# Kernel optimization log

Measured on AMD Instinct MI355X. Metric: run time of the kernel, lower is better.

The kernel has to match this reference:

```python
import jax, jax.numpy as jnp
import numpy as np

B, S, D, H = 2, 2048, 1024, 16
HD = D // H
DFF = 4 * D
EPS = 1e-5


def layernorm(x, g, b):
    mu = jnp.mean(x, axis=-1, keepdims=True)
    var = jnp.mean((x - mu) ** 2, axis=-1, keepdims=True)
    return (x - mu) * jax.lax.rsqrt(var + EPS) * g + b


def setup_inputs() -> dict:
    key = jax.random.key(0)
    ks = jax.random.split(key, 16)
    sc = 0.02
    return {
        "x": jax.random.normal(ks[0], (B, S, D), jnp.float32),
        "pos_emb": jax.random.normal(ks[1], (S, D), jnp.float32),
        "ln1_g": jnp.ones((D,), jnp.float32),
        "ln1_b": jnp.zeros((D,), jnp.float32),
        "w_qkv": jax.random.normal(ks[2], (D, 3 * D), jnp.float32) * sc,
        "b_qkv": jnp.zeros((3 * D,), jnp.float32),
        "w_o": jax.random.normal(ks[3], (D, D), jnp.float32) * sc,
        "b_o": jnp.zeros((D,), jnp.float32),
        "ln2_g": jnp.ones((D,), jnp.float32),
        "ln2_b": jnp.zeros((D,), jnp.float32),
        "w_fc": jax.random.normal(ks[4], (D, DFF), jnp.float32) * sc,
        "b_fc": jnp.zeros((DFF,), jnp.float32),
        "w_proj": jax.random.normal(ks[5], (DFF, D), jnp.float32) * sc,
        "b_proj": jnp.zeros((D,), jnp.float32),
    }


def reference(x, pos_emb, ln1_g, ln1_b, w_qkv, b_qkv, w_o, b_o,
              ln2_g, ln2_b, w_fc, b_fc, w_proj, b_proj):
    # --- attention sub-block: x + attn(norm1(x) + pos_emb) ---
    h = layernorm(x, ln1_g, ln1_b) + pos_emb  # [B,S,D]
    qkv = h @ w_qkv + b_qkv                    # [B,S,3D]
    qkv = qkv.reshape(B, S, 3, H, HD).transpose(2, 0, 3, 1, 4)  # [3,B,H,S,HD]
    q, k, v = qkv[0], qkv[1], qkv[2]
    # naive full attention: materialize [B,H,S,S]
    w = jnp.einsum('bhqd,bhkd->bhqk', q, k) / jnp.sqrt(jnp.float32(HD))
    causal = jnp.tril(jnp.ones((S, S), bool))  # True = keep
    w = jnp.where(causal, w, -jnp.inf)
    a = jax.nn.softmax(w, axis=-1)
    out = jnp.einsum('bhqk,bhkd->bhqd', a, v)   # [B,H,S,HD]
    out = out.transpose(0, 2, 1, 3).reshape(B, S, D)
    x = x + out @ w_o + b_o
    # --- MLP sub-block: x + mlp(norm2(x)) ---
    m = layernorm(x, ln2_g, ln2_b)
    m = jax.nn.gelu(m @ w_fc + b_fc) @ w_proj + b_proj
    return x + m
```

## Files before the change

kernel.cpp:

```cpp
#include <hip/hip_runtime.h>
#include <hip/hip_bf16.h>

typedef __hip_bfloat16 bf16_t;
typedef __bf16 bf16x8 __attribute__((ext_vector_type(8)));
typedef float f32x4 __attribute__((ext_vector_type(4)));

__device__ __forceinline__ void gload_lds16(const void* g, void* l) {
  __builtin_amdgcn_global_load_lds(
      (const __attribute__((address_space(1))) void*)g,
      (__attribute__((address_space(3))) void*)l, 16, 0, 0);
}

__device__ __forceinline__ unsigned short f2bf(float f) {
  bf16_t h = __float2bfloat16(f);
  return reinterpret_cast<unsigned short&>(h);
}

__global__ __launch_bounds__(256) void wtrans_kernel(
    const float* __restrict__ in, bf16_t* __restrict__ out, int K, int N) {
  __shared__ float tile[32][33];
  int tx = threadIdx.x, ty = threadIdx.y;
  int n = blockIdx.x * 32 + tx;
  int k0 = blockIdx.y * 32 + ty;
#pragma unroll
  for (int j = 0; j < 32; j += 8) tile[ty + j][tx] = in[(size_t)(k0 + j) * N + n];
  __syncthreads();
  int k = blockIdx.y * 32 + tx;
  int n0 = blockIdx.x * 32 + ty;
#pragma unroll
  for (int j = 0; j < 32; j += 8)
    out[(size_t)(n0 + j) * K + k] = __float2bfloat16(tile[tx][ty + j]);
}

__global__ __launch_bounds__(256) void ln_kernel(
    const float* __restrict__ x, const float* __restrict__ g,
    const float* __restrict__ b, const float* __restrict__ pos,
    bf16_t* __restrict__ out, int S) {
  int row = blockIdx.x;
  int tid = threadIdx.x;
  const float4* xr = (const float4*)(x + (size_t)row * 1024);
  float4 v = xr[tid];
  float s1 = v.x + v.y + v.z + v.w;
  float s2 = v.x * v.x + v.y * v.y + v.z * v.z + v.w * v.w;
#pragma unroll
  for (int off = 1; off < 64; off <<= 1) {
    s1 += __shfl_xor(s1, off);
    s2 += __shfl_xor(s2, off);
  }
  __shared__ float red[2][4];
  int w = tid >> 6;
  if ((tid & 63) == 0) { red[0][w] = s1; red[1][w] = s2; }
  __syncthreads();
  s1 = red[0][0] + red[0][1] + red[0][2] + red[0][3];
  s2 = red[1][0] + red[1][1] + red[1][2] + red[1][3];
  float mu = s1 * (1.f / 1024.f);
  float var = s2 * (1.f / 1024.f) - mu * mu;
  float rs = rsqrtf(var + 1e-5f);
  float4 gg = ((const float4*)g)[tid];
  float4 bb = ((const float4*)b)[tid];
  float4 pp = {0.f, 0.f, 0.f, 0.f};
  if (pos) pp = ((const float4*)(pos + (size_t)(row & (S - 1)) * 1024))[tid];
  ushort4 o4;
  o4.x = f2bf((v.x - mu) * rs * gg.x + bb.x + pp.x);
  o4.y = f2bf((v.y - mu) * rs * gg.y + bb.y + pp.y);
  o4.z = f2bf((v.z - mu) * rs * gg.z + bb.z + pp.z);
  o4.w = f2bf((v.w - mu) * rs * gg.w + bb.w + pp.w);
  ((ushort4*)(out + (size_t)row * 1024))[tid] = o4;
}

template <int EPI, int DBUF>
__global__ __launch_bounds__(256) void gemm_bt(
    const bf16_t* __restrict__ A, const bf16_t* __restrict__ BT,
    const float* __restrict__ bias, const float* __restrict__ resid,
    float* __restrict__ outf, bf16_t* __restrict__ outb,
    bf16_t* __restrict__ qb, bf16_t* __restrict__ kb, bf16_t* __restrict__ vb,
    int M, int N, int K) {
  __shared__ char lds[DBUF ? 65536 : 32768];
  int tid = threadIdx.x;
  int l = tid & 63;
  int w = tid >> 6;
  int wr = w >> 1, wc = w & 1;
  int ll = l & 15, lg = l >> 4;
  int chunk = gridDim.x >> 3;
  int swz = (blockIdx.x & 7) * chunk + (blockIdx.x >> 3);
  int nbx = N >> 7;
  int bx = swz % nbx, by = swz / nbx;
  int rowBase = by * 128, colBase = bx * 128;

  f32x4 acc[4][4];
  f32x4 z = {0.f, 0.f, 0.f, 0.f};
#pragma unroll
  for (int i = 0; i < 4; i++)
#pragma unroll
    for (int j = 0; j < 4; j++) acc[i][j] = z;

  auto STAGE = [&](int kt, int c) {
#pragma unroll
    for (int i = 0; i < 4; i++) {
      int p = i * 4096 + tid * 16;
      int o = p ^ (((p >> 7) & 7) << 4);
      int r = o >> 7, cc = (o & 127) >> 1;
      gload_lds16(A + (size_t)(rowBase + r) * K + kt * 64 + cc, lds + c * 32768 + p);
    }
#pragma unroll
    for (int i = 0; i < 4; i++) {
      int p = i * 4096 + tid * 16;
      int o = p ^ (((p >> 7) & 7) << 4);
      int r = o >> 7, cc = (o & 127) >> 1;
      gload_lds16(BT + (size_t)(colBase + r) * K + kt * 64 + cc,
                  lds + c * 32768 + 16384 + p);
    }
  };

  int nkt = K >> 6;
  if (DBUF) STAGE(0, 0);
  int cbuf = 0;
  for (int kt = 0; kt < nkt; ++kt) {
    if (DBUF) {
      __builtin_amdgcn_s_barrier();
      if (kt + 1 < nkt) {
        STAGE(kt + 1, cbuf ^ 1);
        asm volatile("s_waitcnt vmcnt(8)" ::: "memory");
      } else {
        asm volatile("s_waitcnt vmcnt(0)" ::: "memory");
      }
      __builtin_amdgcn_s_barrier();
      asm volatile("" ::: "memory");
    } else {
      __syncthreads();
      STAGE(kt, 0);
      __syncthreads();
    }
    char* Ab = lds + cbuf * 32768;
    char* Bb = Ab + 16384;

    bf16x8 af[4][2], bfv[4][2];
#pragma unroll
    for (int mi = 0; mi < 4; mi++) {
      int row = wr * 64 + mi * 16 + ll;
#pragma unroll
      for (int kk = 0; kk < 2; kk++) {
        int o = (row << 7) + (kk << 6) + (lg << 4);
        af[mi][kk] = *(const bf16x8*)(Ab + (o ^ ((row & 7) << 4)));
      }
    }
#pragma unroll
    for (int ni = 0; ni < 4; ni++) {
      int row = wc * 64 + ni * 16 + ll;
#pragma unroll
      for (int kk = 0; kk < 2; kk++) {
        int o = (row << 7) + (kk << 6) + (lg << 4);
        bfv[ni][kk] = *(const bf16x8*)(Bb + (o ^ ((row & 7) << 4)));
      }
    }
#pragma unroll
    for (int mi = 0; mi < 4; mi++)
#pragma unroll
      for (int ni = 0; ni < 4; ni++)
#pragma unroll
        for (int kk = 0; kk < 2; kk++)
          acc[mi][ni] = __builtin_amdgcn_mfma_f32_16x16x32_bf16(
              af[mi][kk], bfv[ni][kk], acc[mi][ni], 0, 0, 0);
    if (DBUF) cbuf ^= 1;
  }

#pragma unroll
  for (int mi = 0; mi < 4; mi++) {
#pragma unroll
    for (int ni = 0; ni < 4; ni++) {
#pragma unroll
      for (int j = 0; j < 4; j++) {
        int grow = rowBase + wr * 64 + mi * 16 + lg * 4 + j;
        int gcol = colBase + wc * 64 + ni * 16 + ll;
        float v = acc[mi][ni][j] + bias[gcol];
        if (EPI == 0) {
          int bb = grow >> 11, s = grow & 2047;
          int t = gcol >> 10, rem = gcol & 1023;
          int h = rem >> 6, d = rem & 63;
          size_t bh = (size_t)(bb * 16 + h);
          if (t == 0)
            qb[(bh * 2048 + s) * 64 + d] = __float2bfloat16(v);
          else if (t == 1)
            kb[(bh * 2048 + s) * 64 + d] = __float2bfloat16(v);
          else
            vb[(bh * 64 + d) * 2048 + s] = __float2bfloat16(v);
        } else if (EPI == 1) {
          size_t idx = (size_t)grow * N + gcol;
          outf[idx] = resid[idx] + v;
        } else {
          float c3 = v * v * v;
          float t = tanhf(0.7978845608028654f * (v + 0.044715f * c3));
          outb[(size_t)grow * N + gcol] = __float2bfloat16(0.5f * v * (1.f + t));
        }
      }
    }
  }
}

__global__ __launch_bounds__(256, 2) void attn_kernel(
    const bf16_t* __restrict__ qb, const bf16_t* __restrict__ kb,
    const bf16_t* __restrict__ vbT, bf16_t* __restrict__ op, int S) {
  int id = blockIdx.x;
  int bh = id & 31;
  int qt = 15 - (id >> 5);
  int tid = threadIdx.x;
  int w = tid >> 6, l = tid & 63;
  int ll = l & 15, lg = l >> 4;
  __shared__ char lds[49152];
  char* Pw = lds + 32768 + w * 4096;

  int qbase = qt * 128;
  int qlo = qbase + w * 32;
  int qhi = qlo + 31;

  bf16x8 qf[2][2];
#pragma unroll
  for (int mi = 0; mi < 2; mi++) {
    const bf16_t* qrp = qb + ((size_t)bh * S + qbase + w * 32 + mi * 16 + ll) * 64;
#pragma unroll
    for (int kk = 0; kk < 2; kk++) qf[mi][kk] = *(const bf16x8*)(qrp + kk * 32 + lg * 8);
  }

  f32x4 Oacc[2][4];
  f32x4 z = {0.f, 0.f, 0.f, 0.f};
#pragma unroll
  for (int mi = 0; mi < 2; mi++)
#pragma unroll
    for (int i = 0; i < 4; i++) Oacc[mi][i] = z;
  float mrow[2], lrow[2];
#pragma unroll
  for (int mi = 0; mi < 2; mi++) { mrow[mi] = -INFINITY; lrow[mi] = 0.f; }

  int last = 2 * qt + 1;

  auto STAGE = [&](int kt, int c) {
    char* Kt = lds + c * 8192;
    char* Vt = lds + 16384 + c * 8192;
#pragma unroll
    for (int i = 0; i < 2; ++i) {
      int p = i * 4096 + tid * 16;
      int o = p ^ (((p >> 7) & 7) << 4);
      int r = o >> 7, cc = (o & 127) >> 1;
      gload_lds16(kb + ((size_t)bh * S + kt * 64 + r) * 64 + cc, Kt + p);
    }
#pragma unroll
    for (int i = 0; i < 2; ++i) {
      int p = i * 4096 + tid * 16;
      int o = p ^ (((p >> 7) & 7) << 4);
      int d = o >> 7, cc = (o & 127) >> 1;
      gload_lds16(vbT + ((size_t)bh * 64 + d) * S + kt * 64 + cc, Vt + p);
    }
  };

  STAGE(0, 0);
  int c = 0;
  for (int kt = 0; kt <= last; ++kt) {
    __builtin_amdgcn_s_barrier();
    if (kt < last) {
      STAGE(kt + 1, c ^ 1);
      asm volatile("s_waitcnt vmcnt(4)" ::: "memory");
    } else {
      asm volatile("s_waitcnt vmcnt(0)" ::: "memory");
    }
    __builtin_amdgcn_s_barrier();
    asm volatile("" ::: "memory");

    if (kt * 64 <= qhi) {
      char* Kt = lds + c * 8192;
      char* Vt = lds + 16384 + c * 8192;

      bf16x8 kf[4][2];
#pragma unroll
      for (int f = 0; f < 4; f++) {
        int row = f * 16 + ll;
#pragma unroll
        for (int kk = 0; kk < 2; kk++) {
          int o = (row << 7) + (kk << 6) + (lg << 4);
          kf[f][kk] = *(const bf16x8*)(Kt + (o ^ ((row & 7) << 4)));
        }
      }
      f32x4 sfr[2][4];
      __builtin_amdgcn_s_setprio(1);
#pragma unroll
      for (int mi = 0; mi < 2; mi++)
#pragma unroll
        for (int f = 0; f < 4; f++) {
          sfr[mi][f] = z;
#pragma unroll
          for (int kk = 0; kk < 2; kk++)
            sfr[mi][f] = __builtin_amdgcn_mfma_f32_16x16x32_bf16(
                kf[f][kk], qf[mi][kk], sfr[mi][f], 0, 0, 0);
        }
      __builtin_amdgcn_s_setprio(0);

      bool diag = (kt * 64 + 63) > qlo;
      float mx[2];
#pragma unroll
      for (int mi = 0; mi < 2; mi++) {
        int gq = qlo + mi * 16 + ll;
        float m_ = -INFINITY;
#pragma unroll
        for (int f = 0; f < 4; f++)
#pragma unroll
          for (int j = 0; j < 4; j++) {
            float s = sfr[mi][f][j] * 0.125f;
            if (diag && (kt * 64 + f * 16 + lg * 4 + j) > gq) s = -INFINITY;
            sfr[mi][f][j] = s;
            m_ = fmaxf(m_, s);
          }
        m_ = fmaxf(m_, __shfl_xor(m_, 16));
        m_ = fmaxf(m_, __shfl_xor(m_, 32));
        mx[mi] = m_;
      }

      bool ok = (mx[0] <= mrow[0] + 8.f) && (mx[1] <= mrow[1] + 8.f);
      if (!__all(ok)) {
#pragma unroll
        for (int mi = 0; mi < 2; mi++) {
          float mnew = fmaxf(mrow[mi], mx[mi]);
          float fj = __expf(mrow[mi] - mnew);
          mrow[mi] = mnew;
          lrow[mi] *= fj;
#pragma unroll
          for (int j = 0; j < 4; j++) {
            float frow = __shfl(fj, (lg << 2) + j);
#pragma unroll
            for (int fd = 0; fd < 4; fd++) Oacc[mi][fd][j] *= frow;
          }
        }
      }

#pragma unroll
      for (int mi = 0; mi < 2; mi++) {
        float sum = 0.f;
        int q = mi * 16 + ll;
#pragma unroll
        for (int f = 0; f < 4; f++) {
          float p0 = __expf(sfr[mi][f][0] - mrow[mi]);
          float p1 = __expf(sfr[mi][f][1] - mrow[mi]);
          float p2 = __expf(sfr[mi][f][2] - mrow[mi]);
          float p3 = __expf(sfr[mi][f][3] - mrow[mi]);
          sum += (p0 + p1) + (p2 + p3);
          uint2 pk;
          pk.x = (unsigned)f2bf(p0) | ((unsigned)f2bf(p1) << 16);
          pk.y = (unsigned)f2bf(p2) | ((unsigned)f2bf(p3) << 16);
          int o = (q << 7) + ((f * 16 + lg * 4) << 1);
          *(uint2*)(Pw + (o ^ ((q & 7) << 4))) = pk;
        }
        sum += __shfl_xor(sum, 16);
        sum += __shfl_xor(sum, 32);
        lrow[mi] += sum;
      }

      bf16x8 vf2[4][2];
#pragma unroll
      for (int fd = 0; fd < 4; fd++) {
        int row = fd * 16 + ll;
#pragma unroll
        for (int kk = 0; kk < 2; kk++) {
          int o = (row << 7) + (kk << 6) + (lg << 4);
          vf2[fd][kk] = *(const bf16x8*)(Vt + (o ^ ((row & 7) << 4)));
        }
      }
      bf16x8 pf[2][2];
#pragma unroll
      for (int mi = 0; mi < 2; mi++) {
        int pr = mi * 16 + ll;
#pragma unroll
        for (int kk = 0; kk < 2; kk++) {
          int o = (pr << 7) + (kk << 6) + (lg << 4);
          pf[mi][kk] = *(const bf16x8*)(Pw + (o ^ ((pr & 7) << 4)));
        }
      }
      __builtin_amdgcn_s_setprio(1);
#pragma unroll
      for (int mi = 0; mi < 2; mi++)
#pragma unroll
        for (int fd = 0; fd < 4; fd++)
#pragma unroll
          for (int kk = 0; kk < 2; kk++)
            Oacc[mi][fd] = __builtin_amdgcn_mfma_f32_16x16x32_bf16(
                pf[mi][kk], vf2[fd][kk], Oacc[mi][fd], 0, 0, 0);
      __builtin_amdgcn_s_setprio(0);
    }
    c ^= 1;
  }

  int b = bh >> 4, hh = bh & 15;
#pragma unroll
  for (int mi = 0; mi < 2; mi++) {
    float invA = 1.f / lrow[mi];
#pragma unroll
    for (int j = 0; j < 4; j++) {
      float inv = __shfl(invA, (lg << 2) + j);
      int srow = qbase + w * 32 + mi * 16 + lg * 4 + j;
#pragma unroll
      for (int fd = 0; fd < 4; fd++) {
        int col = (hh << 6) + (fd << 4) + ll;
        op[((size_t)b * S + srow) * 1024 + col] = __float2bfloat16(Oacc[mi][fd][j] * inv);
      }
    }
  }
}

extern "C" void kernel_launch(void* const* d_in, const int* in_sizes, int n_in,
                              void* d_out, int out_size, void* d_ws, size_t ws_size,
                              hipStream_t stream) {
  const float* x = (const float*)d_in[0];
  const float* pos_emb = (const float*)d_in[1];
  const float* ln1_g = (const float*)d_in[2];
  const float* ln1_b = (const float*)d_in[3];
  const float* w_qkv = (const float*)d_in[4];
  const float* b_qkv = (const float*)d_in[5];
  const float* w_o = (const float*)d_in[6];
  const float* b_o = (const float*)d_in[7];
  const float* ln2_g = (const float*)d_in[8];
  const float* ln2_b = (const float*)d_in[9];
  const float* w_fc = (const float*)d_in[10];
  const float* b_fc = (const float*)d_in[11];
  const float* w_proj = (const float*)d_in[12];
  const float* b_proj = (const float*)d_in[13];

  char* ws = (char*)d_ws;
  auto take = [&](size_t bytes) {
    char* p = ws;
    ws += (bytes + 255) & ~(size_t)255;
    return p;
  };
  bf16_t* wqkvT = (bf16_t*)take(3072ull * 1024 * 2);
  bf16_t* woT = (bf16_t*)take(1024ull * 1024 * 2);
  bf16_t* wfcT = (bf16_t*)take(4096ull * 1024 * 2);
  bf16_t* wprojT = (bf16_t*)take(1024ull * 4096 * 2);
  bf16_t* h = (bf16_t*)take(4096ull * 1024 * 2);
  bf16_t* qbuf = (bf16_t*)take(32ull * 2048 * 64 * 2);
  bf16_t* kbuf = (bf16_t*)take(32ull * 2048 * 64 * 2);
  bf16_t* vbuf = (bf16_t*)take(32ull * 2048 * 64 * 2);
  bf16_t* aout = (bf16_t*)take(4096ull * 1024 * 2);
  float* x2 = (float*)take(4096ull * 1024 * 4);
  bf16_t* mb = (bf16_t*)take(4096ull * 1024 * 2);
  bf16_t* fca = (bf16_t*)qbuf;

  dim3 tb(32, 8);
  wtrans_kernel<<<dim3(3072 / 32, 1024 / 32), tb, 0, stream>>>(w_qkv, wqkvT, 1024, 3072);
  wtrans_kernel<<<dim3(1024 / 32, 1024 / 32), tb, 0, stream>>>(w_o, woT, 1024, 1024);
  wtrans_kernel<<<dim3(4096 / 32, 1024 / 32), tb, 0, stream>>>(w_fc, wfcT, 1024, 4096);
  wtrans_kernel<<<dim3(1024 / 32, 4096 / 32), tb, 0, stream>>>(w_proj, wprojT, 4096, 1024);

  ln_kernel<<<4096, 256, 0, stream>>>(x, ln1_g, ln1_b, pos_emb, h, 2048);

  gemm_bt<0, 0><<<dim3(768), 256, 0, stream>>>(h, wqkvT, b_qkv, nullptr, nullptr,
                                               nullptr, qbuf, kbuf, vbuf, 4096, 3072, 1024);

  attn_kernel<<<dim3(512), 256, 0, stream>>>(qbuf, kbuf, vbuf, aout, 2048);

  gemm_bt<1, 1><<<dim3(256), 256, 0, stream>>>(aout, woT, b_o, x, x2, nullptr,
                                               nullptr, nullptr, nullptr, 4096, 1024, 1024);

  ln_kernel<<<4096, 256, 0, stream>>>(x2, ln2_g, ln2_b, nullptr, mb, 2048);

  gemm_bt<2, 0><<<dim3(1024), 256, 0, stream>>>(mb, wfcT, b_fc, nullptr, nullptr,
                                                fca, nullptr, nullptr, nullptr, 4096, 4096, 1024);

  gemm_bt<1, 1><<<dim3(256), 256, 0, stream>>>(fca, wprojT, b_proj, x2, (float*)d_out,
                                               nullptr, nullptr, nullptr, nullptr, 4096, 1024, 4096);
}
```

Before: 380.5 us.

## Add 256x256-tile double-buffered GEMM for QKV and FC projections

Adds a new 512-thread GEMM kernel that computes 256x256 output tiles from a 128 KB double-buffered LDS with XOR-swizzled direct global-to-LDS loads. It splits next-tile loads across compute phases and raises wave priority around the MFMA blocks. The kernel replaces the 128x128 single-buffered GEMM for the QKV and FC (GELU) projections, aiming for more data reuse per tile and better overlap of loads with compute. The old GEMM keeps only the residual epilogue. The larger tiles mean far fewer blocks (192 and 256), which may underfill the CUs, and the 128 KB LDS per block limits occupancy.

```diff
diff --git a/kernel.cpp b/kernel.cpp
--- a/kernel.cpp
+++ b/kernel.cpp
@@ -68,13 +68,136 @@
   ((ushort4*)(out + (size_t)row * 1024))[tid] = o4;
 }
 
+template <int EPI>
+__global__ __launch_bounds__(512, 2) void gemm256(
+    const bf16_t* __restrict__ A, const bf16_t* __restrict__ BT,
+    const float* __restrict__ bias, bf16_t* __restrict__ outb,
+    bf16_t* __restrict__ qb, bf16_t* __restrict__ kb, bf16_t* __restrict__ vb,
+    int M, int N, int K) {
+  __shared__ char lds[131072];
+  int tid = threadIdx.x;
+  int l = tid & 63, w = tid >> 6;
+  int wr = w >> 2, wc = w & 3;
+  int ll = l & 15, lg = l >> 4;
+  int chunk = gridDim.x >> 3;
+  int swz = (blockIdx.x & 7) * chunk + (blockIdx.x >> 3);
+  int nbx = N >> 8;
+  int bx = swz % nbx, by = swz / nbx;
+  int rowBase = by * 256, colBase = bx * 256;
+
+  f32x4 acc[8][4];
+  f32x4 z = {0.f, 0.f, 0.f, 0.f};
+#pragma unroll
+  for (int i = 0; i < 8; i++)
+#pragma unroll
+    for (int j = 0; j < 4; j++) acc[i][j] = z;
+
+  auto SHALF = [&](int kt, int c, int h) {
+    const bf16_t* src = (h < 2) ? A : BT;
+    int base = (h < 2) ? rowBase : colBase;
+    char* dst = lds + c * 65536 + ((h < 2) ? 0 : 32768);
+    int tileoff = (h & 1) * 16384;
+#pragma unroll
+    for (int i = 0; i < 2; i++) {
+      int p = tileoff + i * 8192 + tid * 16;
+      int o = p ^ (((p >> 7) & 7) << 4);
+      int r = o >> 7, cc = (o & 127) >> 1;
+      gload_lds16(src + (size_t)(base + r) * K + kt * 64 + cc, dst + p);
+    }
+  };
+
+  int nkt = K >> 6;
+#pragma unroll
+  for (int h = 0; h < 4; h++) SHALF(0, 0, h);
+
+  for (int t = 0; t < nkt; ++t) {
+    int c = t & 1;
+    bool more = (t + 1 < nkt);
+    if (more) {
+      SHALF(t + 1, c ^ 1, 0);
+      SHALF(t + 1, c ^ 1, 1);
+      asm volatile("s_waitcnt vmcnt(4)" ::: "memory");
+    } else {
+      asm volatile("s_waitcnt vmcnt(0)" ::: "memory");
+    }
+    __builtin_amdgcn_s_barrier();
+    asm volatile("" ::: "memory");
+    char* Ab = lds + c * 65536;
+    char* Bb = Ab + 32768;
+
+#pragma unroll
+    for (int ph = 0; ph < 4; ++ph) {
+      int mh = ph >> 1, nh = ph & 1;
+      bf16x8 af[4][2], bfv[2][2];
+#pragma unroll
+      for (int q = 0; q < 4; q++) {
+        int row = wr * 128 + (mh * 4 + q) * 16 + ll;
+#pragma unroll
+        for (int kk = 0; kk < 2; kk++) {
+          int o = (row << 7) + (kk << 6) + (lg << 4);
+          af[q][kk] = *(const bf16x8*)(Ab + (o ^ ((row & 7) << 4)));
+        }
+      }
+#pragma unroll
+      for (int n = 0; n < 2; n++) {
+        int row = wc * 64 + (nh * 2 + n) * 16 + ll;
+#pragma unroll
+        for (int kk = 0; kk < 2; kk++) {
+          int o = (row << 7) + (kk << 6) + (lg << 4);
+          bfv[n][kk] = *(const bf16x8*)(Bb + (o ^ ((row & 7) << 4)));
+        }
+      }
+      if (more && ph < 2) SHALF(t + 1, c ^ 1, 2 + ph);
+      __builtin_amdgcn_s_barrier();
+      __builtin_amdgcn_s_setprio(1);
+#pragma unroll
+      for (int q = 0; q < 4; q++)
+#pragma unroll
+        for (int n = 0; n < 2; n++)
+#pragma unroll
+          for (int kk = 0; kk < 2; kk++)
+            acc[mh * 4 + q][nh * 2 + n] = __builtin_amdgcn_mfma_f32_16x16x32_bf16(
+                af[q][kk], bfv[n][kk], acc[mh * 4 + q][nh * 2 + n], 0, 0, 0);
+      __builtin_amdgcn_s_setprio(0);
+      __builtin_amdgcn_s_barrier();
+    }
+  }
+
+#pragma unroll
+  for (int mi = 0; mi < 8; mi++) {
+#pragma unroll
+    for (int ni = 0; ni < 4; ni++) {
+#pragma unroll
+      for (int j = 0; j < 4; j++) {
+        int grow = rowBase + wr * 128 + mi * 16 + lg * 4 + j;
+        int gcol = colBase + wc * 64 + ni * 16 + ll;
+        float v = acc[mi][ni][j] + bias[gcol];
+        if (EPI == 0) {
+          int bb = grow >> 11, s = grow & 2047;
+          int tq = gcol >> 10, rem = gcol & 1023;
+          int h = rem >> 6, d = rem & 63;
+          size_t bh = (size_t)(bb * 16 + h);
+          if (tq == 0)
+            qb[(bh * 2048 + s) * 64 + d] = __float2bfloat16(v);
+          else if (tq == 1)
+            kb[(bh * 2048 + s) * 64 + d] = __float2bfloat16(v);
+          else
+            vb[(bh * 64 + d) * 2048 + s] = __float2bfloat16(v);
+        } else {
+          float c3 = v * v * v;
+          float tt = tanhf(0.7978845608028654f * (v + 0.044715f * c3));
+          outb[(size_t)grow * N + gcol] = __float2bfloat16(0.5f * v * (1.f + tt));
+        }
+      }
+    }
+  }
+}
+
 template <int EPI, int DBUF>
 __global__ __launch_bounds__(256) void gemm_bt(
     const bf16_t* __restrict__ A, const bf16_t* __restrict__ BT,
     const float* __restrict__ bias, const float* __restrict__ resid,
-    float* __restrict__ outf, bf16_t* __restrict__ outb,
-    bf16_t* __restrict__ qb, bf16_t* __restrict__ kb, bf16_t* __restrict__ vb,
-    int M, int N, int K) {
+    float* __restrict__ outf, int M, int N, int K) {
   __shared__ char lds[DBUF ? 65536 : 32768];
   int tid = threadIdx.x;
   int l = tid & 63;
@@ -173,25 +296,8 @@
         int grow = rowBase + wr * 64 + mi * 16 + lg * 4 + j;
         int gcol = colBase + wc * 64 + ni * 16 + ll;
         float v = acc[mi][ni][j] + bias[gcol];
-        if (EPI == 0) {
-          int bb = grow >> 11, s = grow & 2047;
-          int t = gcol >> 10, rem = gcol & 1023;
-          int h = rem >> 6, d = rem & 63;
-          size_t bh = (size_t)(bb * 16 + h);
-          if (t == 0)
-            qb[(bh * 2048 + s) * 64 + d] = __float2bfloat16(v);
-          else if (t == 1)
-            kb[(bh * 2048 + s) * 64 + d] = __float2bfloat16(v);
-          else
-            vb[(bh * 64 + d) * 2048 + s] = __float2bfloat16(v);
-        } else if (EPI == 1) {
-          size_t idx = (size_t)grow * N + gcol;
-          outf[idx] = resid[idx] + v;
-        } else {
-          float c3 = v * v * v;
-          float t = tanhf(0.7978845608028654f * (v + 0.044715f * c3));
-          outb[(size_t)grow * N + gcol] = __float2bfloat16(0.5f * v * (1.f + t));
-        }
+        size_t idx = (size_t)grow * N + gcol;
+        outf[idx] = resid[idx] + v;
       }
     }
   }
@@ -448,19 +554,19 @@
 
   ln_kernel<<<4096, 256, 0, stream>>>(x, ln1_g, ln1_b, pos_emb, h, 2048);
 
-  gemm_bt<0, 0><<<dim3(768), 256, 0, stream>>>(h, wqkvT, b_qkv, nullptr, nullptr,
-                                               nullptr, qbuf, kbuf, vbuf, 4096, 3072, 1024);
+  gemm256<0><<<dim3(192), 512, 0, stream>>>(h, wqkvT, b_qkv, nullptr,
+                                            qbuf, kbuf, vbuf, 4096, 3072, 1024);
 
   attn_kernel<<<dim3(512), 256, 0, stream>>>(qbuf, kbuf, vbuf, aout, 2048);
 
-  gemm_bt<1, 1><<<dim3(256), 256, 0, stream>>>(aout, woT, b_o, x, x2, nullptr,
-                                               nullptr, nullptr, nullptr, 4096, 1024, 1024);
+  gemm_bt<1, 1><<<dim3(256), 256, 0, stream>>>(aout, woT, b_o, x, x2,
+                                               4096, 1024, 1024);
 
   ln_kernel<<<4096, 256, 0, stream>>>(x2, ln2_g, ln2_b, nullptr, mb, 2048);
 
-  gemm_bt<2, 0><<<dim3(1024), 256, 0, stream>>>(mb, wfcT, b_fc, nullptr, nullptr,
-                                                fca, nullptr, nullptr, nullptr, 4096, 4096, 1024);
+  gemm256<2><<<dim3(256), 512, 0, stream>>>(mb, wfcT, b_fc, fca,
+                                            nullptr, nullptr, nullptr, 4096, 4096, 1024);
 
   gemm_bt<1, 1><<<dim3(256), 256, 0, stream>>>(fca, wprojT, b_proj, x2, (float*)d_out,
-                                               nullptr, nullptr, nullptr, nullptr, 4096, 1024, 4096);
-}
+                                               4096, 1024, 4096);
+}
```

Result: no change. 385.8 us (+1.4%).
